# Performance work log

Hardware: AMD Instinct MI355X
Metric: run time of the kernel (lower is better)

## Reference

```python
import jax, jax.numpy as jnp
import numpy as np

N_HEAD = 12

def setup_inputs() -> dict:
    key = jax.random.key(0)
    k1, k2, k3 = jax.random.split(key, 3)
    B, T, E = 4, 2048, 768
    x = jax.random.normal(k1, (B, T, E), dtype=jnp.float32)
    Wqkv = jax.random.normal(k2, (E, 3 * E), dtype=jnp.float32) * 0.02
    Wproj = jax.random.normal(k3, (E, E), dtype=jnp.float32) * 0.02
    return {"x": x, "Wqkv": Wqkv, "Wproj": Wproj}

def reference(x, Wqkv, Wproj):
    B, T, E = x.shape
    H = N_HEAD
    hd = E // H
    qkv = x @ Wqkv                                  # [B,T,3E]
    q, k, v = jnp.split(qkv, 3, axis=-1)
    # [B,T,E] -> [B,H,T,hd]
    q = q.reshape(B, T, H, hd).transpose(0, 2, 1, 3)
    k = k.reshape(B, T, H, hd).transpose(0, 2, 1, 3)
    v = v.reshape(B, T, H, hd).transpose(0, 2, 1, 3)
    scores = jnp.einsum("bhqd,bhkd->bhqk", q, k) / jnp.sqrt(jnp.float32(hd))
    # original: masked_fill(tril(scores)==0, -inf) == causal mask (upper triangle zeroed by tril)
    masked = jnp.where(jnp.tril(scores) == 0, -jnp.inf, scores)
    attn = jax.nn.softmax(masked, axis=-1)
    out = jnp.einsum("bhqk,bhkd->bhqd", attn, v)    # [B,H,T,hd]
    out = out.transpose(0, 2, 1, 3).reshape(B, T, E)
    return out @ Wproj
```

## Files before the change

kernel.cpp:

```cpp
#include <hip/hip_runtime.h>
#include <hip/hip_bf16.h>


#define BB 4
#define TT 2048
#define EE 768
#define HH 12
#define HD 64
#define KK 768
#define BTE (BB*TT*EE)

typedef __attribute__((ext_vector_type(8))) short bf16x8;
typedef __attribute__((ext_vector_type(4))) float f32x4;
typedef __attribute__((ext_vector_type(16))) float f32x16;
typedef __attribute__((ext_vector_type(4))) int i32x4;

#define QSC 0.18033688011112042f

#define GLOAD16(gp, lp) \
    __builtin_amdgcn_global_load_lds( \
        (const __attribute__((address_space(1))) unsigned*)(gp), \
        (__attribute__((address_space(3))) unsigned*)(lp), 16, 0, 0)

static __device__ __forceinline__ unsigned short f2bf(float f) {
    unsigned u = __builtin_bit_cast(unsigned, f);
    u += 0x7fffu + ((u >> 16) & 1u);
    return (unsigned short)(u >> 16);
}

static __device__ __forceinline__ unsigned cvt_pk_bf16(float lo, float hi) {
    unsigned r;
    asm("v_cvt_pk_bf16_f32 %0, %1, %2" : "=v"(r) : "v"(lo), "v"(hi));
    return r;
}

__global__ __launch_bounds__(256)
void convx_kernel(const float* __restrict__ x, unsigned short* __restrict__ xf) {
    const int t16 = blockIdx.x;
    const int tid = threadIdx.x;
    const int l = tid & 63;
    const int row = t16 * 16 + (l & 15);
    const int kbase = (l >> 4) << 3;
#pragma unroll
    for (int pass = 0; pass < 6; ++pass) {
        const int kb = (tid >> 6) + 4 * pass;
        const int k = kb * 32 + kbase;
        float4 a = *(const float4*)&x[(size_t)row * KK + k];
        float4 b = *(const float4*)&x[(size_t)row * KK + k + 4];
        ushort4 lo, hi;
        lo.x = f2bf(a.x); lo.y = f2bf(a.y); lo.z = f2bf(a.z); lo.w = f2bf(a.w);
        hi.x = f2bf(b.x); hi.y = f2bf(b.y); hi.z = f2bf(b.z); hi.w = f2bf(b.w);
        unsigned short* dst = &xf[((size_t)t16 * 24 + kb) * 512 + l * 8];
        *(ushort4*)dst = lo;
        *(ushort4*)(dst + 4) = hi;
    }
}

__global__ __launch_bounds__(256)
void transw_kernel(const float* __restrict__ W, unsigned short* __restrict__ Wf, int N) {
    __shared__ unsigned short Ts[64][72];
    const int n0 = blockIdx.x * 64;
    const int k0 = blockIdx.y * 64;
    const int tid = threadIdx.x;
    {
        const int r = tid >> 4;
        const int c4 = (tid & 15) << 2;
#pragma unroll
        for (int i = 0; i < 4; ++i) {
            const int k = r + i * 16;
            float4 w4 = *(const float4*)&W[(size_t)(k0 + k) * N + n0 + c4];
            Ts[k][c4 + 0] = f2bf(w4.x); Ts[k][c4 + 1] = f2bf(w4.y);
            Ts[k][c4 + 2] = f2bf(w4.z); Ts[k][c4 + 3] = f2bf(w4.w);
        }
    }
    __syncthreads();
#pragma unroll
    for (int i = 0; i < 2; ++i) {
        const int idx = tid + i * 256;
        const int sub = idx >> 6;
        const int l = idx & 63;
        const int n16l = sub & 3, kbl = sub >> 2;
        const int nloc = n16l * 16 + (l & 15);
        const int kloc = kbl * 32 + ((l >> 4) << 3);
        ushort4 p0, p1;
        p0.x = Ts[kloc + 0][nloc]; p0.y = Ts[kloc + 1][nloc];
        p0.z = Ts[kloc + 2][nloc]; p0.w = Ts[kloc + 3][nloc];
        p1.x = Ts[kloc + 4][nloc]; p1.y = Ts[kloc + 5][nloc];
        p1.z = Ts[kloc + 6][nloc]; p1.w = Ts[kloc + 7][nloc];
        const int n16 = (n0 >> 4) + n16l;
        const int kb  = (k0 >> 5) + kbl;
        unsigned short* dst = &Wf[((size_t)n16 * 24 + kb) * 512 + l * 8];
        *(ushort4*)dst = p0;
        *(ushort4*)(dst + 4) = p1;
    }
}

template<int MODE>
__global__ __launch_bounds__(256)
void mfma_gemm_kernel(const unsigned short* __restrict__ Af,
                      const unsigned short* __restrict__ Bf,
                      unsigned short* __restrict__ q_ws,
                      unsigned short* __restrict__ k_ws,
                      unsigned short* __restrict__ v_ws,
                      float* __restrict__ outf) {
    __shared__ __align__(16) unsigned short As[3][8 * 512];
    __shared__ __align__(16) unsigned short Bs[3][8 * 512];

    const int nwg = gridDim.x * gridDim.y;
    const int orig = blockIdx.y * gridDim.x + blockIdx.x;
    const int cpx = nwg >> 3;
    const int swz = (orig & 7) * cpx + (orig >> 3);
    const int bx = swz % gridDim.x;
    const int by = swz / gridDim.x;

    const int tid = threadIdx.x;
    const int w = tid >> 6, lane = tid & 63;
    const int c = lane & 15, g = lane >> 4;
    const int wr = w >> 1, wc = w & 1;
    const int m0 = by * 128, n0 = bx * 128;

    const unsigned short* Ap = Af + ((size_t)(m0 >> 4) * 24) * 512;
    const unsigned short* Bp = Bf + ((size_t)(n0 >> 4) * 24) * 512;

    f32x4 acc[4][4] = {};
    const int NT = KK / 32;

#define GSTAGE(pp, kt_) do { const int f0_ = 2 * w; \
        GLOAD16(Ap + ((size_t)(f0_    ) * 24 + (kt_)) * 512 + lane * 8, &As[pp][(f0_    ) * 512]); \
        GLOAD16(Ap + ((size_t)(f0_ + 1) * 24 + (kt_)) * 512 + lane * 8, &As[pp][(f0_ + 1) * 512]); \
        GLOAD16(Bp + ((size_t)(f0_    ) * 24 + (kt_)) * 512 + lane * 8, &Bs[pp][(f0_    ) * 512]); \
        GLOAD16(Bp + ((size_t)(f0_ + 1) * 24 + (kt_)) * 512 + lane * 8, &Bs[pp][(f0_ + 1) * 512]); \
    } while (0)

    GSTAGE(0, 0);
    GSTAGE(1, 1);

    for (int kt = 0; kt < NT; ++kt) {
        if (kt < NT - 1) asm volatile("s_waitcnt vmcnt(4)" ::: "memory");
        else             asm volatile("s_waitcnt vmcnt(0)" ::: "memory");
        __builtin_amdgcn_s_barrier();
        __builtin_amdgcn_sched_barrier(0);
        asm volatile("" ::: "memory");

        if (kt + 2 < NT) GSTAGE((kt + 2) % 3, kt + 2);

        const int p = kt % 3;
        bf16x8 af[4], bfr[4];
#pragma unroll
        for (int m = 0; m < 4; ++m)
            af[m] = *(const bf16x8*)&As[p][(wr * 4 + m) * 512 + lane * 8];
#pragma unroll
        for (int n = 0; n < 4; ++n)
            bfr[n] = *(const bf16x8*)&Bs[p][(wc * 4 + n) * 512 + lane * 8];
        __builtin_amdgcn_s_setprio(1);
#pragma unroll
        for (int m = 0; m < 4; ++m)
#pragma unroll
            for (int n = 0; n < 4; ++n)
                acc[m][n] = __builtin_amdgcn_mfma_f32_16x16x32_bf16(af[m], bfr[n], acc[m][n], 0, 0, 0);
        __builtin_amdgcn_s_setprio(0);
    }
#undef GSTAGE

    if (MODE == 0) {
        const int which = n0 / EE;
        const int hh = (n0 % EE) / HD + wc;
        const int bb = m0 / TT;
        const int tb = (m0 % TT) + wr * 64;
        const int bh = bb * HH + hh;
        if (which < 2) {
            const float sc_ = (which == 0) ? QSC : 1.0f;
            unsigned short* dst = (which == 0) ? q_ws : k_ws;
#pragma unroll
            for (int m = 0; m < 4; ++m) {
                const int t32 = (tb >> 5) + (m >> 1);
#pragma unroll
                for (int n = 0; n < 4; ++n) {
                    unsigned short* base = dst
                        + ((size_t)(bh * (TT / 32) + t32) * 4 + n) * 512
                        + ((m & 1) * 16 + 4 * g + 32 * (c >> 3)) * 8 + (c & 7);
#pragma unroll
                    for (int j = 0; j < 4; ++j)
                        base[j * 8] = f2bf(acc[m][n][j] * sc_);
                }
            }
        } else {
            unsigned short* vb = v_ws + ((size_t)(bh * (TT / 64) + (tb >> 6))) * 4096;
#pragma unroll
            for (int m = 0; m < 4; ++m)
#pragma unroll
                for (int n = 0; n < 4; ++n) {
                    unsigned short* base = vb + ((size_t)(n >> 1) * 4 + m) * 512
                        + ((n & 1) * 16 + c + 32 * (g >> 1)) * 8 + 4 * (g & 1);
                    ushort4 pk;
                    pk.x = f2bf(acc[m][n][0]); pk.y = f2bf(acc[m][n][1]);
                    pk.z = f2bf(acc[m][n][2]); pk.w = f2bf(acc[m][n][3]);
                    *(ushort4*)base = pk;
                }
        }
    } else {
#pragma unroll
        for (int m = 0; m < 4; ++m)
#pragma unroll
            for (int n = 0; n < 4; ++n)
#pragma unroll
                for (int j = 0; j < 4; ++j)
                    outf[(size_t)(m0 + wr * 64 + m * 16 + 4 * g + j) * EE
                         + n0 + wc * 64 + n * 16 + c] = acc[m][n][j];
    }
}

__global__ __launch_bounds__(256)
void attn_kernel(const unsigned short* __restrict__ qf,
                 const unsigned short* __restrict__ kfr,
                 const unsigned short* __restrict__ vfr,
                 unsigned short* __restrict__ attn_f) {
    const int bh = blockIdx.x;
    const int wv = threadIdx.x >> 6;
    const int j = (TT / 32 - 1) - ((int)blockIdx.y * 4 + wv);
    const int b = bh / HH, h = bh % HH;
    const int lane = threadIdx.x & 63;
    const int lq = lane & 31;
    const int hiL = lane >> 5;

    const int q0 = j * 32;
    const int qg = q0 + lq;

    const unsigned short* qbase = qf + ((size_t)(bh * (TT / 32) + j)) * 2048;
    bf16x8 qa[4];
#pragma unroll
    for (int ds = 0; ds < 4; ++ds)
        qa[ds] = *(const bf16x8*)&qbase[ds * 512 + lane * 8];

    const unsigned short* kfb = kfr + (size_t)bh * 131072;
    const unsigned short* vfb = vfr + (size_t)bh * 131072;

    const i32x4 onesw = {0x3F803F80, 0x3F803F80, 0x3F803F80, 0x3F803F80};
    const bf16x8 ones = __builtin_bit_cast(bf16x8, onesw);

    f32x16 o0 = {}, o1 = {}, ol = {};

    const int ktiles = (j >> 1) + 1;

    for (int kt = 0; kt < ktiles; ++kt) {
        const int kv0 = kt * 64;

        bf16x8 kf[8], vf[8];
        {
            const unsigned short* kc = kfb + ((size_t)(2 * kt) * 4) * 512 + lane * 8;
#pragma unroll
            for (int ch = 0; ch < 8; ++ch)
                kf[ch] = *(const bf16x8*)&kc[ch * 512];
            const unsigned short* vc = vfb + (size_t)kt * 4096 + lane * 8;
#pragma unroll
            for (int ch = 0; ch < 8; ++ch)
                vf[ch] = *(const bf16x8*)&vc[ch * 512];
        }

        f32x16 s0 = {}, s1 = {};
        __builtin_amdgcn_s_setprio(1);
#pragma unroll
        for (int ds = 0; ds < 4; ++ds) {
            s0 = __builtin_amdgcn_mfma_f32_32x32x16_bf16(kf[ds],     qa[ds], s0, 0, 0, 0);
            s1 = __builtin_amdgcn_mfma_f32_32x32x16_bf16(kf[4 + ds], qa[ds], s1, 0, 0, 0);
        }
        __builtin_amdgcn_s_setprio(0);

        if (kv0 + 63 > q0) {
#pragma unroll
            for (int r = 0; r < 16; ++r) {
                const int crow = (r & 3) + 8 * (r >> 2) + 4 * hiL;
                if (kv0 + crow > qg)      s0[r] = -INFINITY;
                if (kv0 + 32 + crow > qg) s1[r] = -INFINITY;
            }
        }

#pragma unroll
        for (int r = 0; r < 16; ++r) s0[r] = __builtin_amdgcn_exp2f(s0[r]);
#pragma unroll
        for (int r = 0; r < 16; ++r) s1[r] = __builtin_amdgcn_exp2f(s1[r]);

        __builtin_amdgcn_s_setprio(1);
#define PACKSTEP(E0,E1,E2,E3,E4,E5,E6,E7, VK) do { \
        unsigned a0 = cvt_pk_bf16(E0, E1); \
        unsigned a1 = cvt_pk_bf16(E2, E3); \
        unsigned b0 = cvt_pk_bf16(E4, E5); \
        unsigned b1 = cvt_pk_bf16(E6, E7); \
        asm("v_permlane32_swap_b32 %0, %1" : "+v"(a0), "+v"(b0)); \
        asm("v_permlane32_swap_b32 %0, %1" : "+v"(a1), "+v"(b1)); \
        i32x4 pw; \
        pw[0] = (int)a0; pw[1] = (int)a1; pw[2] = (int)b0; pw[3] = (int)b1; \
        const bf16x8 pa = __builtin_bit_cast(bf16x8, pw); \
        o0 = __builtin_amdgcn_mfma_f32_32x32x16_bf16(pa, vf[VK],     o0, 0, 0, 0); \
        o1 = __builtin_amdgcn_mfma_f32_32x32x16_bf16(pa, vf[4 + VK], o1, 0, 0, 0); \
        ol = __builtin_amdgcn_mfma_f32_32x32x16_bf16(pa, ones,       ol, 0, 0, 0); \
    } while (0)

        PACKSTEP(s0[0], s0[1], s0[2], s0[3], s0[4], s0[5], s0[6], s0[7], 0);
        PACKSTEP(s0[8], s0[9], s0[10], s0[11], s0[12], s0[13], s0[14], s0[15], 1);
        PACKSTEP(s1[0], s1[1], s1[2], s1[3], s1[4], s1[5], s1[6], s1[7], 2);
        PACKSTEP(s1[8], s1[9], s1[10], s1[11], s1[12], s1[13], s1[14], s1[15], 3);
#undef PACKSTEP
        __builtin_amdgcn_s_setprio(0);
    }

    const int rbase = b * TT + q0;
#pragma unroll
    for (int r = 0; r < 16; ++r) {
        const int crow = (r & 3) + 8 * (r >> 2) + 4 * hiL;
        const float li = 1.f / ol[r];
        const int t16 = (rbase + crow) >> 4;
        const int lA = (crow & 15) + 16 * (lq >> 3);
        const int e  = lq & 7;
        attn_f[((size_t)t16 * 24 + (h * 2 + 0)) * 512 + lA * 8 + e] = f2bf(o0[r] * li);
        attn_f[((size_t)t16 * 24 + (h * 2 + 1)) * 512 + lA * 8 + e] = f2bf(o1[r] * li);
    }
}

extern "C" void kernel_launch(void* const* d_in, const int* in_sizes, int n_in,
                              void* d_out, int out_size, void* d_ws, size_t ws_size,
                              hipStream_t stream) {
    const float* x     = (const float*)d_in[0];
    const float* wqkv  = (const float*)d_in[1];
    const float* wproj = (const float*)d_in[2];
    float* out = (float*)d_out;

    unsigned short* ws = (unsigned short*)d_ws;
    unsigned short* q_ws    = ws;
    unsigned short* k_ws    = ws + (size_t)BTE;
    unsigned short* v_ws    = ws + 2 * (size_t)BTE;
    unsigned short* xf      = ws + 3 * (size_t)BTE;
    unsigned short* attn_f  = ws + 4 * (size_t)BTE;
    unsigned short* wqkv_f  = ws + 5 * (size_t)BTE;
    unsigned short* wproj_f = wqkv_f + (size_t)2304 * 768;

    convx_kernel<<<TT * BB / 16, 256, 0, stream>>>(x, xf);
    transw_kernel<<<dim3(2304 / 64, KK / 64), 256, 0, stream>>>(wqkv, wqkv_f, 2304);
    transw_kernel<<<dim3(768 / 64, KK / 64), 256, 0, stream>>>(wproj, wproj_f, 768);

    mfma_gemm_kernel<0><<<dim3(2304 / 128, 8192 / 128), 256, 0, stream>>>(
        xf, wqkv_f, q_ws, k_ws, v_ws, nullptr);
    attn_kernel<<<dim3(BB * HH, TT / 128), 256, 0, stream>>>(q_ws, k_ws, v_ws, attn_f);
    mfma_gemm_kernel<1><<<dim3(EE / 128, 8192 / 128), 256, 0, stream>>>(
        attn_f, wproj_f, nullptr, nullptr, nullptr, out);
}
```

Before: 121.0 us.

## Stage shared K/V tiles in LDS with triple-buffered async global loads

The attention kernel previously had each wave read its K and V fragments straight from global memory every tile. Now the four waves cooperatively load each 64-key K/V tile into a triple-buffered LDS ring using global_load_lds, prefetching two tiles ahead with waitcnt plus barrier synchronisation. The query-block assignment is remapped so the four waves in a block hold consecutive query tiles, which lets them share the loaded keys. Waves skip compute on tiles beyond their causal limit but still take part in the barriers. This trades duplicated global/L2 traffic for LDS usage and a per-tile block barrier, which can stall waves with uneven causal work.

```diff
diff --git a/kernel.cpp b/kernel.cpp
--- a/kernel.cpp
+++ b/kernel.cpp
@@ -215,9 +215,12 @@
                  const unsigned short* __restrict__ kfr,
                  const unsigned short* __restrict__ vfr,
                  unsigned short* __restrict__ attn_f) {
+    __shared__ __align__(16) unsigned short KVs[3][16 * 512];
+
     const int bh = blockIdx.x;
     const int wv = threadIdx.x >> 6;
-    const int j = (TT / 32 - 1) - ((int)blockIdx.y * 4 + wv);
+    const int yy = 15 - (int)blockIdx.y;
+    const int j = 4 * yy + wv;
     const int b = bh / HH, h = bh % HH;
     const int lane = threadIdx.x & 63;
     const int lq = lane & 31;
@@ -240,69 +243,92 @@
 
     f32x16 o0 = {}, o1 = {}, ol = {};
 
-    const int ktiles = (j >> 1) + 1;
-
-    for (int kt = 0; kt < ktiles; ++kt) {
+    const int NTb = 2 * yy + 2;
+
+#define STAGE(pp, kt_) do { \
+        if (wv < 2) { const int c0_ = wv * 4; \
+            GLOAD16(kfb + ((size_t)(2 * (kt_)) * 4 + c0_ + 0) * 512 + lane * 8, &KVs[pp][(c0_ + 0) * 512]); \
+            GLOAD16(kfb + ((size_t)(2 * (kt_)) * 4 + c0_ + 1) * 512 + lane * 8, &KVs[pp][(c0_ + 1) * 512]); \
+            GLOAD16(kfb + ((size_t)(2 * (kt_)) * 4 + c0_ + 2) * 512 + lane * 8, &KVs[pp][(c0_ + 2) * 512]); \
+            GLOAD16(kfb + ((size_t)(2 * (kt_)) * 4 + c0_ + 3) * 512 + lane * 8, &KVs[pp][(c0_ + 3) * 512]); \
+        } else { const int c0_ = (wv - 2) * 4; \
+            GLOAD16(vfb + (size_t)(kt_) * 4096 + (c0_ + 0) * 512 + lane * 8, &KVs[pp][(8 + c0_ + 0) * 512]); \
+            GLOAD16(vfb + (size_t)(kt_) * 4096 + (c0_ + 1) * 512 + lane * 8, &KVs[pp][(8 + c0_ + 1) * 512]); \
+            GLOAD16(vfb + (size_t)(kt_) * 4096 + (c0_ + 2) * 512 + lane * 8, &KVs[pp][(8 + c0_ + 2) * 512]); \
+            GLOAD16(vfb + (size_t)(kt_) * 4096 + (c0_ + 3) * 512 + lane * 8, &KVs[pp][(8 + c0_ + 3) * 512]); \
+        } } while (0)
+
+    STAGE(0, 0);
+    if (NTb > 1) STAGE(1, 1);
+
+    for (int kt = 0; kt < NTb; ++kt) {
+        if (kt < NTb - 1) asm volatile("s_waitcnt vmcnt(4)" ::: "memory");
+        else              asm volatile("s_waitcnt vmcnt(0)" ::: "memory");
+        __builtin_amdgcn_s_barrier();
+        __builtin_amdgcn_sched_barrier(0);
+        asm volatile("" ::: "memory");
+
+        if (kt + 2 < NTb) STAGE((kt + 2) % 3, kt + 2);
+
         const int kv0 = kt * 64;
-
-        bf16x8 kf[8], vf[8];
-        {
-            const unsigned short* kc = kfb + ((size_t)(2 * kt) * 4) * 512 + lane * 8;
+        if (kv0 <= q0 + 31) {
+            const int p = kt % 3;
+            bf16x8 kf[8], vf[8];
 #pragma unroll
             for (int ch = 0; ch < 8; ++ch)
-                kf[ch] = *(const bf16x8*)&kc[ch * 512];
-            const unsigned short* vc = vfb + (size_t)kt * 4096 + lane * 8;
+                kf[ch] = *(const bf16x8*)&KVs[p][ch * 512 + lane * 8];
 #pragma unroll
             for (int ch = 0; ch < 8; ++ch)
-                vf[ch] = *(const bf16x8*)&vc[ch * 512];
+                vf[ch] = *(const bf16x8*)&KVs[p][(8 + ch) * 512 + lane * 8];
+
+            f32x16 s0 = {}, s1 = {};
+            __builtin_amdgcn_s_setprio(1);
+#pragma unroll
+            for (int ds = 0; ds < 4; ++ds) {
+                s0 = __builtin_amdgcn_mfma_f32_32x32x16_bf16(kf[ds],     qa[ds], s0, 0, 0, 0);
+                s1 = __builtin_amdgcn_mfma_f32_32x32x16_bf16(kf[4 + ds], qa[ds], s1, 0, 0, 0);
+            }
+            __builtin_amdgcn_s_setprio(0);
+
+            if (kv0 + 63 > q0) {
+#pragma unroll
+                for (int r = 0; r < 16; ++r) {
+                    const int crow = (r & 3) + 8 * (r >> 2) + 4 * hiL;
+                    if (kv0 + crow > qg)      s0[r] = -INFINITY;
+                    if (kv0 + 32 + crow > qg) s1[r] = -INFINITY;
+                }
+            }
+
+#pragma unroll
+            for (int r = 0; r < 16; ++r) s0[r] = __builtin_amdgcn_exp2f(s0[r]);
+#pragma unroll
+            for (int r = 0; r < 16; ++r) s1[r] = __builtin_amdgcn_exp2f(s1[r]);
+
+            __builtin_amdgcn_s_setprio(1);
+#define PACKSTEP(E0,E1,E2,E3,E4,E5,E6,E7, VK) do { \
+            unsigned a0 = cvt_pk_bf16(E0, E1); \
+            unsigned a1 = cvt_pk_bf16(E2, E3); \
+            unsigned b0 = cvt_pk_bf16(E4, E5); \
+            unsigned b1 = cvt_pk_bf16(E6, E7); \
+            asm("v_permlane32_swap_b32 %0, %1" : "+v"(a0), "+v"(b0)); \
+            asm("v_permlane32_swap_b32 %0, %1" : "+v"(a1), "+v"(b1)); \
+            i32x4 pw; \
+            pw[0] = (int)a0; pw[1] = (int)a1; pw[2] = (int)b0; pw[3] = (int)b1; \
+            const bf16x8 pa = __builtin_bit_cast(bf16x8, pw); \
+            o0 = __builtin_amdgcn_mfma_f32_32x32x16_bf16(pa, vf[VK],     o0, 0, 0, 0); \
+            o1 = __builtin_amdgcn_mfma_f32_32x32x16_bf16(pa, vf[4 + VK], o1, 0, 0, 0); \
+            ol = __builtin_amdgcn_mfma_f32_32x32x16_bf16(pa, ones,       ol, 0, 0, 0); \
+        } while (0)
+
+            PACKSTEP(s0[0], s0[1], s0[2], s0[3], s0[4], s0[5], s0[6], s0[7], 0);
+            PACKSTEP(s0[8], s0[9], s0[10], s0[11], s0[12], s0[13], s0[14], s0[15], 1);
+            PACKSTEP(s1[0], s1[1], s1[2], s1[3], s1[4], s1[5], s1[6], s1[7], 2);
+            PACKSTEP(s1[8], s1[9], s1[10], s1[11], s1[12], s1[13], s1[14], s1[15], 3);
+#undef PACKSTEP
+            __builtin_amdgcn_s_setprio(0);
         }
-
-        f32x16 s0 = {}, s1 = {};
-        __builtin_amdgcn_s_setprio(1);
-#pragma unroll
-        for (int ds = 0; ds < 4; ++ds) {
-            s0 = __builtin_amdgcn_mfma_f32_32x32x16_bf16(kf[ds],     qa[ds], s0, 0, 0, 0);
-            s1 = __builtin_amdgcn_mfma_f32_32x32x16_bf16(kf[4 + ds], qa[ds], s1, 0, 0, 0);
-        }
-        __builtin_amdgcn_s_setprio(0);
-
-        if (kv0 + 63 > q0) {
-#pragma unroll
-            for (int r = 0; r < 16; ++r) {
-                const int crow = (r & 3) + 8 * (r >> 2) + 4 * hiL;
-                if (kv0 + crow > qg)      s0[r] = -INFINITY;
-                if (kv0 + 32 + crow > qg) s1[r] = -INFINITY;
-            }
-        }
-
-#pragma unroll
-        for (int r = 0; r < 16; ++r) s0[r] = __builtin_amdgcn_exp2f(s0[r]);
-#pragma unroll
-        for (int r = 0; r < 16; ++r) s1[r] = __builtin_amdgcn_exp2f(s1[r]);
-
-        __builtin_amdgcn_s_setprio(1);
-#define PACKSTEP(E0,E1,E2,E3,E4,E5,E6,E7, VK) do { \
-        unsigned a0 = cvt_pk_bf16(E0, E1); \
-        unsigned a1 = cvt_pk_bf16(E2, E3); \
-        unsigned b0 = cvt_pk_bf16(E4, E5); \
-        unsigned b1 = cvt_pk_bf16(E6, E7); \
-        asm("v_permlane32_swap_b32 %0, %1" : "+v"(a0), "+v"(b0)); \
-        asm("v_permlane32_swap_b32 %0, %1" : "+v"(a1), "+v"(b1)); \
-        i32x4 pw; \
-        pw[0] = (int)a0; pw[1] = (int)a1; pw[2] = (int)b0; pw[3] = (int)b1; \
-        const bf16x8 pa = __builtin_bit_cast(bf16x8, pw); \
-        o0 = __builtin_amdgcn_mfma_f32_32x32x16_bf16(pa, vf[VK],     o0, 0, 0, 0); \
-        o1 = __builtin_amdgcn_mfma_f32_32x32x16_bf16(pa, vf[4 + VK], o1, 0, 0, 0); \
-        ol = __builtin_amdgcn_mfma_f32_32x32x16_bf16(pa, ones,       ol, 0, 0, 0); \
-    } while (0)
-
-        PACKSTEP(s0[0], s0[1], s0[2], s0[3], s0[4], s0[5], s0[6], s0[7], 0);
-        PACKSTEP(s0[8], s0[9], s0[10], s0[11], s0[12], s0[13], s0[14], s0[15], 1);
-        PACKSTEP(s1[0], s1[1], s1[2], s1[3], s1[4], s1[5], s1[6], s1[7], 2);
-        PACKSTEP(s1[8], s1[9], s1[10], s1[11], s1[12], s1[13], s1[14], s1[15], 3);
-#undef PACKSTEP
-        __builtin_amdgcn_s_setprio(0);
-    }
+    }
+#undef STAGE
 
     const int rbase = b * TT + q0;
 #pragma unroll
```

After: 124.7 us. 3.0% more time.

## Process two query tiles per wave to reuse K/V fragments in attention

Applied to the files above, without the earlier changes.

Each wave now handles two adjacent 32-row query tiles, sharing every K and V fragment load between both. Blocks shrink to 128 threads, with the grid adjusted so the same number of query tiles is covered. The goal is to halve per-tile global K/V load traffic and give the scheduler more independent MFMA work. In exchange, register pressure roughly doubles for the accumulators and there are fewer waves in flight, which could hurt occupancy and latency hiding.

```diff
diff --git a/kernel.cpp b/kernel.cpp
--- a/kernel.cpp
+++ b/kernel.cpp
@@ -210,27 +210,32 @@
     }
 }
 
-__global__ __launch_bounds__(256)
+__global__ __launch_bounds__(128)
 void attn_kernel(const unsigned short* __restrict__ qf,
                  const unsigned short* __restrict__ kfr,
                  const unsigned short* __restrict__ vfr,
                  unsigned short* __restrict__ attn_f) {
     const int bh = blockIdx.x;
     const int wv = threadIdx.x >> 6;
-    const int j = (TT / 32 - 1) - ((int)blockIdx.y * 4 + wv);
+    const int yy = 15 - (int)blockIdx.y;
+    const int pr = 2 * yy + wv;
+    const int jA = 2 * pr, jB = 2 * pr + 1;
     const int b = bh / HH, h = bh % HH;
     const int lane = threadIdx.x & 63;
     const int lq = lane & 31;
     const int hiL = lane >> 5;
 
-    const int q0 = j * 32;
-    const int qg = q0 + lq;
-
-    const unsigned short* qbase = qf + ((size_t)(bh * (TT / 32) + j)) * 2048;
-    bf16x8 qa[4];
-#pragma unroll
-    for (int ds = 0; ds < 4; ++ds)
-        qa[ds] = *(const bf16x8*)&qbase[ds * 512 + lane * 8];
+    const int q0A = jA * 32, q0B = jB * 32;
+    const int qgA = q0A + lq, qgB = q0B + lq;
+
+    const unsigned short* qbA = qf + ((size_t)(bh * (TT / 32) + jA)) * 2048;
+    const unsigned short* qbB = qf + ((size_t)(bh * (TT / 32) + jB)) * 2048;
+    bf16x8 qaA[4], qaB[4];
+#pragma unroll
+    for (int ds = 0; ds < 4; ++ds) {
+        qaA[ds] = *(const bf16x8*)&qbA[ds * 512 + lane * 8];
+        qaB[ds] = *(const bf16x8*)&qbB[ds * 512 + lane * 8];
+    }
 
     const unsigned short* kfb = kfr + (size_t)bh * 131072;
     const unsigned short* vfb = vfr + (size_t)bh * 131072;
@@ -238,83 +243,120 @@
     const i32x4 onesw = {0x3F803F80, 0x3F803F80, 0x3F803F80, 0x3F803F80};
     const bf16x8 ones = __builtin_bit_cast(bf16x8, onesw);
 
-    f32x16 o0 = {}, o1 = {}, ol = {};
-
-    const int ktiles = (j >> 1) + 1;
+    f32x16 o0A = {}, o1A = {}, olA = {};
+    f32x16 o0B = {}, o1B = {}, olB = {};
+
+    const int ktiles = pr + 1;
+
+#define PACKW(S0_, S1_, IDX_, DST_) do { \
+        unsigned a0 = cvt_pk_bf16(S0_[IDX_ + 0], S0_[IDX_ + 1]); \
+        unsigned a1 = cvt_pk_bf16(S0_[IDX_ + 2], S0_[IDX_ + 3]); \
+        unsigned b0 = cvt_pk_bf16(S0_[IDX_ + 4], S0_[IDX_ + 5]); \
+        unsigned b1 = cvt_pk_bf16(S0_[IDX_ + 6], S0_[IDX_ + 7]); \
+        asm("v_permlane32_swap_b32 %0, %1" : "+v"(a0), "+v"(b0)); \
+        asm("v_permlane32_swap_b32 %0, %1" : "+v"(a1), "+v"(b1)); \
+        DST_[0] = (int)a0; DST_[1] = (int)a1; DST_[2] = (int)b0; DST_[3] = (int)b1; \
+    } while (0)
+
+#define SMPACK(Q0_, QG_, PW_) do { \
+        if (kv0 + 63 > (Q0_)) { \
+            _Pragma("unroll") \
+            for (int r = 0; r < 16; ++r) { \
+                const int crow = (r & 3) + 8 * (r >> 2) + 4 * hiL; \
+                if (kv0 + crow > (QG_))      s0[r] = -INFINITY; \
+                if (kv0 + 32 + crow > (QG_)) s1[r] = -INFINITY; \
+            } \
+        } \
+        _Pragma("unroll") \
+        for (int r = 0; r < 16; ++r) s0[r] = __builtin_amdgcn_exp2f(s0[r]); \
+        _Pragma("unroll") \
+        for (int r = 0; r < 16; ++r) s1[r] = __builtin_amdgcn_exp2f(s1[r]); \
+        PACKW(s0, s0, 0, PW_[0]); \
+        PACKW(s0, s0, 8, PW_[1]); \
+        PACKW(s1, s1, 0, PW_[2]); \
+        PACKW(s1, s1, 8, PW_[3]); \
+    } while (0)
 
     for (int kt = 0; kt < ktiles; ++kt) {
         const int kv0 = kt * 64;
 
-        bf16x8 kf[8], vf[8];
+        bf16x8 kf[8];
         {
             const unsigned short* kc = kfb + ((size_t)(2 * kt) * 4) * 512 + lane * 8;
 #pragma unroll
             for (int ch = 0; ch < 8; ++ch)
                 kf[ch] = *(const bf16x8*)&kc[ch * 512];
+        }
+
+        i32x4 pwA[4], pwB[4];
+
+        {
+            f32x16 s0 = {}, s1 = {};
+            __builtin_amdgcn_s_setprio(1);
+#pragma unroll
+            for (int ds = 0; ds < 4; ++ds) {
+                s0 = __builtin_amdgcn_mfma_f32_32x32x16_bf16(kf[ds],     qaA[ds], s0, 0, 0, 0);
+                s1 = __builtin_amdgcn_mfma_f32_32x32x16_bf16(kf[4 + ds], qaA[ds], s1, 0, 0, 0);
+            }
+            __builtin_amdgcn_s_setprio(0);
+            SMPACK(q0A, qgA, pwA);
+        }
+        {
+            f32x16 s0 = {}, s1 = {};
+            __builtin_amdgcn_s_setprio(1);
+#pragma unroll
+            for (int ds = 0; ds < 4; ++ds) {
+                s0 = __builtin_amdgcn_mfma_f32_32x32x16_bf16(kf[ds],     qaB[ds], s0, 0, 0, 0);
+                s1 = __builtin_amdgcn_mfma_f32_32x32x16_bf16(kf[4 + ds], qaB[ds], s1, 0, 0, 0);
+            }
+            __builtin_amdgcn_s_setprio(0);
+            SMPACK(q0B, qgB, pwB);
+        }
+
+        bf16x8 vf[8];
+        {
             const unsigned short* vc = vfb + (size_t)kt * 4096 + lane * 8;
 #pragma unroll
             for (int ch = 0; ch < 8; ++ch)
                 vf[ch] = *(const bf16x8*)&vc[ch * 512];
         }
 
-        f32x16 s0 = {}, s1 = {};
         __builtin_amdgcn_s_setprio(1);
 #pragma unroll
-        for (int ds = 0; ds < 4; ++ds) {
-            s0 = __builtin_amdgcn_mfma_f32_32x32x16_bf16(kf[ds],     qa[ds], s0, 0, 0, 0);
-            s1 = __builtin_amdgcn_mfma_f32_32x32x16_bf16(kf[4 + ds], qa[ds], s1, 0, 0, 0);
+        for (int ks = 0; ks < 4; ++ks) {
+            const bf16x8 paA = __builtin_bit_cast(bf16x8, pwA[ks]);
+            o0A = __builtin_amdgcn_mfma_f32_32x32x16_bf16(paA, vf[ks],     o0A, 0, 0, 0);
+            o1A = __builtin_amdgcn_mfma_f32_32x32x16_bf16(paA, vf[4 + ks], o1A, 0, 0, 0);
+            olA = __builtin_amdgcn_mfma_f32_32x32x16_bf16(paA, ones,       olA, 0, 0, 0);
+        }
+#pragma unroll
+        for (int ks = 0; ks < 4; ++ks) {
+            const bf16x8 paB = __builtin_bit_cast(bf16x8, pwB[ks]);
+            o0B = __builtin_amdgcn_mfma_f32_32x32x16_bf16(paB, vf[ks],     o0B, 0, 0, 0);
+            o1B = __builtin_amdgcn_mfma_f32_32x32x16_bf16(paB, vf[4 + ks], o1B, 0, 0, 0);
+            olB = __builtin_amdgcn_mfma_f32_32x32x16_bf16(paB, ones,       olB, 0, 0, 0);
         }
         __builtin_amdgcn_s_setprio(0);
-
-        if (kv0 + 63 > q0) {
-#pragma unroll
-            for (int r = 0; r < 16; ++r) {
-                const int crow = (r & 3) + 8 * (r >> 2) + 4 * hiL;
-                if (kv0 + crow > qg)      s0[r] = -INFINITY;
-                if (kv0 + 32 + crow > qg) s1[r] = -INFINITY;
-            }
-        }
-
-#pragma unroll
-        for (int r = 0; r < 16; ++r) s0[r] = __builtin_amdgcn_exp2f(s0[r]);
-#pragma unroll
-        for (int r = 0; r < 16; ++r) s1[r] = __builtin_amdgcn_exp2f(s1[r]);
-
-        __builtin_amdgcn_s_setprio(1);
-#define PACKSTEP(E0,E1,E2,E3,E4,E5,E6,E7, VK) do { \
-        unsigned a0 = cvt_pk_bf16(E0, E1); \
-        unsigned a1 = cvt_pk_bf16(E2, E3); \
-        unsigned b0 = cvt_pk_bf16(E4, E5); \
-        unsigned b1 = cvt_pk_bf16(E6, E7); \
-        asm("v_permlane32_swap_b32 %0, %1" : "+v"(a0), "+v"(b0)); \
-        asm("v_permlane32_swap_b32 %0, %1" : "+v"(a1), "+v"(b1)); \
-        i32x4 pw; \
-        pw[0] = (int)a0; pw[1] = (int)a1; pw[2] = (int)b0; pw[3] = (int)b1; \
-        const bf16x8 pa = __builtin_bit_cast(bf16x8, pw); \
-        o0 = __builtin_amdgcn_mfma_f32_32x32x16_bf16(pa, vf[VK],     o0, 0, 0, 0); \
-        o1 = __builtin_amdgcn_mfma_f32_32x32x16_bf16(pa, vf[4 + VK], o1, 0, 0, 0); \
-        ol = __builtin_amdgcn_mfma_f32_32x32x16_bf16(pa, ones,       ol, 0, 0, 0); \
-    } while (0)
-
-        PACKSTEP(s0[0], s0[1], s0[2], s0[3], s0[4], s0[5], s0[6], s0[7], 0);
-        PACKSTEP(s0[8], s0[9], s0[10], s0[11], s0[12], s0[13], s0[14], s0[15], 1);
-        PACKSTEP(s1[0], s1[1], s1[2], s1[3], s1[4], s1[5], s1[6], s1[7], 2);
-        PACKSTEP(s1[8], s1[9], s1[10], s1[11], s1[12], s1[13], s1[14], s1[15], 3);
-#undef PACKSTEP
-        __builtin_amdgcn_s_setprio(0);
-    }
-
-    const int rbase = b * TT + q0;
-#pragma unroll
-    for (int r = 0; r < 16; ++r) {
-        const int crow = (r & 3) + 8 * (r >> 2) + 4 * hiL;
-        const float li = 1.f / ol[r];
-        const int t16 = (rbase + crow) >> 4;
-        const int lA = (crow & 15) + 16 * (lq >> 3);
-        const int e  = lq & 7;
-        attn_f[((size_t)t16 * 24 + (h * 2 + 0)) * 512 + lA * 8 + e] = f2bf(o0[r] * li);
-        attn_f[((size_t)t16 * 24 + (h * 2 + 1)) * 512 + lA * 8 + e] = f2bf(o1[r] * li);
-    }
+    }
+#undef SMPACK
+#undef PACKW
+
+#define EPI(Q0_, O0_, O1_, OL_) do { \
+        const int rbase = b * TT + (Q0_); \
+        _Pragma("unroll") \
+        for (int r = 0; r < 16; ++r) { \
+            const int crow = (r & 3) + 8 * (r >> 2) + 4 * hiL; \
+            const float li = 1.f / OL_[r]; \
+            const int t16 = (rbase + crow) >> 4; \
+            const int lA = (crow & 15) + 16 * (lq >> 3); \
+            const int e  = lq & 7; \
+            attn_f[((size_t)t16 * 24 + (h * 2 + 0)) * 512 + lA * 8 + e] = f2bf(O0_[r] * li); \
+            attn_f[((size_t)t16 * 24 + (h * 2 + 1)) * 512 + lA * 8 + e] = f2bf(O1_[r] * li); \
+        } } while (0)
+
+    EPI(q0A, o0A, o1A, olA);
+    EPI(q0B, o0B, o1B, olB);
+#undef EPI
 }
 
 extern "C" void kernel_launch(void* const* d_in, const int* in_sizes, int n_in,
@@ -340,7 +382,7 @@
 
     mfma_gemm_kernel<0><<<dim3(2304 / 128, 8192 / 128), 256, 0, stream>>>(
         xf, wqkv_f, q_ws, k_ws, v_ws, nullptr);
-    attn_kernel<<<dim3(BB * HH, TT / 128), 256, 0, stream>>>(q_ws, k_ws, v_ws, attn_f);
+    attn_kernel<<<dim3(BB * HH, 16), 128, 0, stream>>>(q_ws, k_ws, v_ws, attn_f);
     mfma_gemm_kernel<1><<<dim3(EE / 128, 8192 / 128), 256, 0, stream>>>(
         attn_f, wproj_f, nullptr, nullptr, nullptr, out);
 }
```

Result: slower. 136.0 us (+12.3%).
